# Kernel optimization log

Measured on AMD Instinct MI355X. Metric: run time of the kernel, lower is better.

Reference implementation:

```python
import jax, jax.numpy as jnp
import numpy as np

B, N, DIM = 4, 2048, 512
HEADS, DIM_HEAD = 8, 64
HID = HEADS * DIM_HEAD


def setup_inputs() -> dict:
    key = jax.random.key(0)
    k1, k2, k3, k4, k5 = jax.random.split(key, 5)
    x = jax.random.normal(k1, (B, N, DIM), jnp.float32)
    pos_bias = jax.random.normal(k2, (HEADS, N, N), jnp.float32) * 0.02
    focus_present_mask = jax.random.bernoulli(k3, 0.5, (B,))
    w_qkv = jax.random.normal(k4, (DIM, 3 * HID), jnp.float32) * (DIM ** -0.5)
    w_out = jax.random.normal(k5, (HID, DIM), jnp.float32) * (HID ** -0.5)
    return {"x": x, "pos_bias": pos_bias, "focus_present_mask": focus_present_mask,
            "w_qkv": w_qkv, "w_out": w_out}


def reference(x, pos_bias, focus_present_mask, w_qkv, w_out):
    scale = DIM_HEAD ** -0.5
    qkv = x @ w_qkv                                   # (B, N, 3*HID)
    q, k, v = jnp.split(qkv, 3, axis=-1)

    def to_heads(t):  # (B, N, HID) -> (B, H, N, D)
        return t.reshape(B, N, HEADS, DIM_HEAD).transpose(0, 2, 1, 3)

    q = to_heads(q) * scale
    k = to_heads(k)
    v = to_heads(v)

    sim = jnp.einsum('bhid,bhjd->bhij', q, k) + pos_bias[None]  # (B, H, N, N)

    # focus_present_mask[b] True -> attend only to self (eye); False -> attend all
    eye = jnp.eye(N, dtype=bool)
    mask = jnp.where(focus_present_mask[:, None, None, None],
                     eye[None, None], jnp.bool_(True))          # (B,1,N,N)
    sim = jnp.where(mask, sim, -jnp.finfo(sim.dtype).max)

    attn = jax.nn.softmax(sim, axis=-1)  # stable softmax == subtract-max + softmax
    out = jnp.einsum('bhij,bhjd->bhid', attn, v)
    out = out.transpose(0, 2, 1, 3).reshape(B, N, HID)
    return out @ w_out
```

## Files before the change

kernel.cpp:

```cpp
#include <hip/hip_runtime.h>
#include <hip/hip_bf16.h>
#include <float.h>

#define B_   4
#define N_   2048
#define DIM_ 512
#define H_   8
#define DH_  64

typedef unsigned short ushort;
typedef __attribute__((ext_vector_type(8))) short short8;
typedef __attribute__((ext_vector_type(4))) float f32x4;

__device__ __forceinline__ ushort f2bf(float f) {
    union { float f; unsigned u; } v; v.f = f;
    return (ushort)((v.u + 0x7fffu + ((v.u >> 16) & 1u)) >> 16);
}
__device__ __forceinline__ float bf2f(ushort u) {
    union { unsigned u; float f; } v; v.u = ((unsigned)u) << 16;
    return v.f;
}

typedef const __attribute__((address_space(1))) unsigned int* gas_t;
typedef __attribute__((address_space(3))) unsigned int* las_t;
__device__ __forceinline__ void gl_lds16(const void* g, void* l) {
    __builtin_amdgcn_global_load_lds((gas_t)g, (las_t)l, 16, 0, 0);
}

__global__ __launch_bounds__(256) void prep_kernel(
    const float* __restrict__ x, const float* __restrict__ wqkv,
    const float* __restrict__ wo,
    ushort* __restrict__ xb, ushort* __restrict__ wqkvT, ushort* __restrict__ woT)
{
    __shared__ ushort tile[64][72];
    const int bx = blockIdx.x;
    const int t = threadIdx.x;
    if (bx < 2048) {
        int gid = bx * 256 + t;
        const float4* xv = (const float4*)x;
        float4 v0 = xv[gid * 2], v1 = xv[gid * 2 + 1];
        uint4 pk;
        pk.x = (unsigned)f2bf(v0.x) | ((unsigned)f2bf(v0.y) << 16);
        pk.y = (unsigned)f2bf(v0.z) | ((unsigned)f2bf(v0.w) << 16);
        pk.z = (unsigned)f2bf(v1.x) | ((unsigned)f2bf(v1.y) << 16);
        pk.w = (unsigned)f2bf(v1.z) | ((unsigned)f2bf(v1.w) << 16);
        ((uint4*)xb)[gid] = pk;
        return;
    }
    int bi = bx - 2048;
    const float* src; ushort* dst; int C, tc, tr;
    if (bi < 192) { src = wqkv; dst = wqkvT; C = 1536; tc = bi % 24; tr = bi / 24; }
    else { bi -= 192; src = wo; dst = woT; C = 512; tc = bi & 7; tr = bi >> 3; }

    const int row = t >> 2, c16 = (t & 3) * 16;
    const float* sp = src + (size_t)(tr * 64 + row) * C + tc * 64 + c16;
    #pragma unroll
    for (int i = 0; i < 4; ++i) {
        float4 v = ((const float4*)sp)[i];
        tile[row][c16 + i * 4 + 0] = f2bf(v.x);
        tile[row][c16 + i * 4 + 1] = f2bf(v.y);
        tile[row][c16 + i * 4 + 2] = f2bf(v.z);
        tile[row][c16 + i * 4 + 3] = f2bf(v.w);
    }
    __syncthreads();
    ushort s[16];
    #pragma unroll
    for (int i = 0; i < 16; ++i) s[i] = tile[c16 + i][row];
    ushort* dp = dst + (size_t)(tc * 64 + row) * 512 + tr * 64 + c16;
    *(uint4*)dp       = *(uint4*)&s[0];
    *(uint4*)(dp + 8) = *(uint4*)&s[8];
}

__global__ __launch_bounds__(256) void qkv_gemm(
    const ushort* __restrict__ A, const ushort* __restrict__ Bt,
    const int* __restrict__ mask,
    ushort* __restrict__ qb, ushort* __restrict__ kb, ushort* __restrict__ vb,
    ushort* __restrict__ vT)
{
    __shared__ ushort sA[128 * 64];
    __shared__ ushort sB[128 * 64];
    const int bn = blockIdx.x;
    const int bm = blockIdx.y;
    if (bn < 8 && mask[bm >> 4] != 0) return;

    const int t = threadIdx.x, w_id = t >> 6, lane = t & 63;
    const int l15 = lane & 15, quad = lane >> 4;
    const int mo = (w_id & 1) * 64, no = (w_id >> 1) * 64;
    const int lr = lane >> 3, lc = (lane & 7) * 8;

    f32x4 acc[4][4] = {};

    for (int kt = 0; kt < 8; ++kt) {
        __syncthreads();
        #pragma unroll
        for (int i = 0; i < 4; ++i) {
            int j = w_id * 4 + i;
            gl_lds16(A  + (size_t)(bm * 128 + j * 8 + lr) * 512 + kt * 64 + lc, &sA[j * 512]);
            gl_lds16(Bt + (size_t)(bn * 128 + j * 8 + lr) * 512 + kt * 64 + lc, &sB[j * 512]);
        }
        __syncthreads();
        #pragma unroll
        for (int c = 0; c < 2; ++c) {
            short8 af[4], bf[4];
            #pragma unroll
            for (int mt = 0; mt < 4; ++mt)
                af[mt] = *(const short8*)&sA[(mo + mt * 16 + l15) * 64 + c * 32 + quad * 8];
            #pragma unroll
            for (int n2 = 0; n2 < 4; ++n2)
                bf[n2] = *(const short8*)&sB[(no + n2 * 16 + l15) * 64 + c * 32 + quad * 8];
            #pragma unroll
            for (int mt = 0; mt < 4; ++mt)
                #pragma unroll
                for (int n2 = 0; n2 < 4; ++n2)
                    acc[mt][n2] = __builtin_amdgcn_mfma_f32_16x16x32_bf16(af[mt], bf[n2], acc[mt][n2], 0, 0, 0);
        }
    }

    const int gn0 = bn * 128 + no;
    const int which = gn0 >> 9;
    const int h = (gn0 >> 6) & 7;
    ushort* dst = which == 0 ? qb : (which == 1 ? kb : vb);
    const float sc = which == 0 ? 0.125f : 1.0f;
    #pragma unroll
    for (int mt = 0; mt < 4; ++mt) {
        const int m0 = bm * 128 + mo + mt * 16 + quad * 4;
        #pragma unroll
        for (int n2 = 0; n2 < 4; ++n2) {
            int d = n2 * 16 + l15;
            ushort w0, w1, w2, w3;
            #pragma unroll
            for (int r = 0; r < 4; ++r) {
                int m = m0 + r, b = m >> 11, n = m & 2047;
                ushort bfv = f2bf(acc[mt][n2][r] * sc);
                dst[((size_t)(b * 8 + h) * 2048 + n) * 64 + d] = bfv;
                if (r == 0) w0 = bfv; else if (r == 1) w1 = bfv;
                else if (r == 2) w2 = bfv; else w3 = bfv;
            }
            if (which == 2) {
                int b = m0 >> 11, n0 = m0 & 2047;
                uint2 pk;
                pk.x = (unsigned)w0 | ((unsigned)w1 << 16);
                pk.y = (unsigned)w2 | ((unsigned)w3 << 16);
                *(uint2*)&vT[((size_t)(b * 8 + h) * 64 + d) * 2048 + n0] = pk;
            }
        }
    }
}

__global__ __launch_bounds__(256) void attn_kernel(
    const ushort* __restrict__ qg, const ushort* __restrict__ kg,
    const ushort* __restrict__ vTg, const float* __restrict__ bias,
    const int* __restrict__ mask,
    ushort* __restrict__ po, float* __restrict__ pl)
{
    const int bid = blockIdx.x;
    const int qblk = bid & 31, s = (bid >> 5) & 1, h = (bid >> 6) & 7, b = bid >> 9;
    if (mask[b] != 0) return;

    const int t = threadIdx.x, w_id = t >> 6, lane = t & 63;
    const int l15 = lane & 15, quad = lane >> 4;
    const int lr = lane >> 3, lc = (lane & 7) * 8;
    const int bh = b * 8 + h;
    const int kbase = s * 1024;

    __shared__ ushort lds_k[64 * 64];
    __shared__ ushort lds_vt[64 * 64];
    __shared__ ushort lds_sp[4 * 16 * 68];

    const ushort* kptr = kg  + (size_t)bh * 2048 * 64;
    const ushort* vtp  = vTg + (size_t)bh * 64 * 2048;

    const ushort* qrp = qg + (size_t)bh * 2048 * 64 + (size_t)(qblk * 64 + w_id * 16 + l15) * 64;
    short8 qf0 = *(const short8*)(qrp + quad * 8);
    short8 qf1 = *(const short8*)(qrp + 32 + quad * 8);

    const int qrow0 = qblk * 64 + w_id * 16 + quad * 4;
    const float* bp = bias + ((size_t)h * 2048 + qrow0) * 2048 + kbase;

    float breg[16];
    #pragma unroll
    for (int tt = 0; tt < 4; ++tt)
        #pragma unroll
        for (int r = 0; r < 4; ++r)
            breg[tt * 4 + r] = bp[(size_t)r * 2048 + tt * 16 + l15];

    f32x4 o[4] = {};
    float lsum[4] = {0.f, 0.f, 0.f, 0.f};

    for (int it = 0; it < 16; ++it) {
        __syncthreads();
        #pragma unroll
        for (int i = 0; i < 2; ++i) {
            int j = w_id * 2 + i;
            gl_lds16(kptr + (size_t)(kbase + it * 64 + j * 8 + lr) * 64 + lc, &lds_k[j * 512]);
            gl_lds16(vtp + (size_t)(j * 8 + lr) * 2048 + kbase + it * 64 + lc, &lds_vt[j * 512]);
        }
        __syncthreads();

        f32x4 sv[4] = {};
        #pragma unroll
        for (int tt = 0; tt < 4; ++tt) {
            short8 kf0 = *(const short8*)&lds_k[(tt * 16 + l15) * 64 + quad * 8];
            short8 kf1 = *(const short8*)&lds_k[(tt * 16 + l15) * 64 + 32 + quad * 8];
            sv[tt] = __builtin_amdgcn_mfma_f32_16x16x32_bf16(qf0, kf0, sv[tt], 0, 0, 0);
            sv[tt] = __builtin_amdgcn_mfma_f32_16x16x32_bf16(qf1, kf1, sv[tt], 0, 0, 0);
        }
        #pragma unroll
        for (int tt = 0; tt < 4; ++tt)
            #pragma unroll
            for (int r = 0; r < 4; ++r)
                sv[tt][r] += breg[tt * 4 + r];

        if (it < 15) {
            #pragma unroll
            for (int tt = 0; tt < 4; ++tt)
                #pragma unroll
                for (int r = 0; r < 4; ++r)
                    breg[tt * 4 + r] = bp[(size_t)r * 2048 + (it + 1) * 64 + tt * 16 + l15];
        }

        const int prow0 = (w_id * 16 + quad * 4) * 68;
        #pragma unroll
        for (int r = 0; r < 4; ++r) {
            float e0 = __expf(sv[0][r]), e1 = __expf(sv[1][r]);
            float e2 = __expf(sv[2][r]), e3 = __expf(sv[3][r]);
            lsum[r] += (e0 + e1) + (e2 + e3);
            const int pr = prow0 + r * 68;
            lds_sp[pr + l15]      = f2bf(e0);
            lds_sp[pr + 16 + l15] = f2bf(e1);
            lds_sp[pr + 32 + l15] = f2bf(e2);
            lds_sp[pr + 48 + l15] = f2bf(e3);
        }

        asm volatile("s_waitcnt lgkmcnt(0)" ::: "memory");

        short8 pf0 = *(const short8*)&lds_sp[(w_id * 16 + l15) * 68 + quad * 8];
        short8 pf1 = *(const short8*)&lds_sp[(w_id * 16 + l15) * 68 + 32 + quad * 8];
        #pragma unroll
        for (int nt = 0; nt < 4; ++nt) {
            short8 vf0 = *(const short8*)&lds_vt[(nt * 16 + l15) * 64 + quad * 8];
            short8 vf1 = *(const short8*)&lds_vt[(nt * 16 + l15) * 64 + 32 + quad * 8];
            o[nt] = __builtin_amdgcn_mfma_f32_16x16x32_bf16(pf0, vf0, o[nt], 0, 0, 0);
            o[nt] = __builtin_amdgcn_mfma_f32_16x16x32_bf16(pf1, vf1, o[nt], 0, 0, 0);
        }
    }

    #pragma unroll
    for (int r = 0; r < 4; ++r) {
        #pragma unroll
        for (int off = 1; off < 16; off <<= 1)
            lsum[r] += __shfl_xor(lsum[r], off, 64);
    }

    #pragma unroll
    for (int r = 0; r < 4; ++r) {
        const int qrow = qrow0 + r;
        const size_t base = ((size_t)(s * 32 + bh) * 2048 + qrow) * 64;
        #pragma unroll
        for (int nt = 0; nt < 4; ++nt)
            po[base + nt * 16 + l15] = f2bf(o[nt][r]);
        if (l15 == 0)
            pl[(size_t)(s * 32 + bh) * 2048 + qrow] = lsum[r];
    }
}

__global__ __launch_bounds__(256) void combine_kernel(
    const ushort* __restrict__ po, const float* __restrict__ pl,
    const ushort* __restrict__ vb, const int* __restrict__ mask,
    ushort* __restrict__ ob)
{
    const int gid = blockIdx.x * 256 + threadIdx.x;
    const int dd = (gid & 7) * 8;
    const int h = (gid >> 3) & 7, n = (gid >> 6) & 2047, b = gid >> 17;
    const int bh = b * 8 + h;
    ushort* op = ob + ((size_t)b * 2048 + n) * 512 + h * 64 + dd;
    if (mask[b] != 0) {
        *(uint4*)op = *(const uint4*)(vb + ((size_t)bh * 2048 + n) * 64 + dd);
        return;
    }
    const size_t i1 = (size_t)bh * 2048 + n;
    const size_t i2 = (size_t)(32 + bh) * 2048 + n;
    float inv = 1.f / (pl[i1] + pl[i2]);
    uint4 ua = *(const uint4*)(po + i1 * 64 + dd);
    uint4 ub = *(const uint4*)(po + i2 * 64 + dd);
    const ushort* pa = (const ushort*)&ua;
    const ushort* pb = (const ushort*)&ub;
    ushort res[8];
    #pragma unroll
    for (int j = 0; j < 8; ++j)
        res[j] = f2bf((bf2f(pa[j]) + bf2f(pb[j])) * inv);
    *(uint4*)op = *(uint4*)res;
}

__global__ __launch_bounds__(256) void out_gemm(
    const ushort* __restrict__ A, const ushort* __restrict__ Bt,
    float* __restrict__ out)
{
    __shared__ ushort sA[2][128 * 64];
    __shared__ ushort sB[2][128 * 64];
    const int bn = blockIdx.x;
    const int bm = blockIdx.y;
    const int t = threadIdx.x, w_id = t >> 6, lane = t & 63;
    const int l15 = lane & 15, quad = lane >> 4;
    const int mo = (w_id & 1) * 64, no = (w_id >> 1) * 64;
    const int lr = lane >> 3;
    const int lcs = ((lane & 7) ^ lr) * 8;
    const int rsw = l15 & 7;

    f32x4 acc[4][4] = {};

    #pragma unroll
    for (int i = 0; i < 4; ++i) {
        int j = w_id * 4 + i;
        gl_lds16(A  + (size_t)(bm * 128 + j * 8 + lr) * 512 + lcs, &sA[0][j * 512]);
        gl_lds16(Bt + (size_t)(bn * 128 + j * 8 + lr) * 512 + lcs, &sB[0][j * 512]);
    }
    asm volatile("s_waitcnt vmcnt(0)" ::: "memory");
    __syncthreads();

    for (int kt = 0; kt < 8; ++kt) {
        const int cur = kt & 1;
        if (kt + 1 < 8) {
            #pragma unroll
            for (int i = 0; i < 4; ++i) {
                int j = w_id * 4 + i;
                gl_lds16(A  + (size_t)(bm * 128 + j * 8 + lr) * 512 + (kt + 1) * 64 + lcs,
                         &sA[cur ^ 1][j * 512]);
                gl_lds16(Bt + (size_t)(bn * 128 + j * 8 + lr) * 512 + (kt + 1) * 64 + lcs,
                         &sB[cur ^ 1][j * 512]);
            }
        }
        #pragma unroll
        for (int c = 0; c < 2; ++c) {
            short8 af[4], bf[4];
            #pragma unroll
            for (int mt = 0; mt < 4; ++mt)
                af[mt] = *(const short8*)&sA[cur][(mo + mt * 16 + l15) * 64 + (((c * 4 + quad) ^ rsw)) * 8];
            #pragma unroll
            for (int n2 = 0; n2 < 4; ++n2)
                bf[n2] = *(const short8*)&sB[cur][(no + n2 * 16 + l15) * 64 + (((c * 4 + quad) ^ rsw)) * 8];
            #pragma unroll
            for (int mt = 0; mt < 4; ++mt)
                #pragma unroll
                for (int n2 = 0; n2 < 4; ++n2)
                    acc[mt][n2] = __builtin_amdgcn_mfma_f32_16x16x32_bf16(af[mt], bf[n2], acc[mt][n2], 0, 0, 0);
        }
        asm volatile("s_waitcnt vmcnt(0)" ::: "memory");
        __syncthreads();
    }
    #pragma unroll
    for (int mt = 0; mt < 4; ++mt) {
        const int m0 = bm * 128 + mo + mt * 16 + quad * 4;
        #pragma unroll
        for (int n2 = 0; n2 < 4; ++n2) {
            int col = bn * 128 + no + n2 * 16 + l15;
            #pragma unroll
            for (int r = 0; r < 4; ++r)
                out[(size_t)(m0 + r) * 512 + col] = acc[mt][n2][r];
        }
    }
}

extern "C" void kernel_launch(void* const* d_in, const int* in_sizes, int n_in,
                              void* d_out, int out_size, void* d_ws, size_t ws_size,
                              hipStream_t stream)
{
    const float* x        = (const float*)d_in[0];
    const float* pos_bias = (const float*)d_in[1];
    const int*   mask     = (const int*)d_in[2];
    const float* w_qkv    = (const float*)d_in[3];
    const float* w_out    = (const float*)d_in[4];
    float* out = (float*)d_out;

    char* ws = (char*)d_ws;
    ushort* qb    = (ushort*)(ws + 0);
    ushort* kb    = (ushort*)(ws + 8388608);
    ushort* vb    = (ushort*)(ws + 16777216);
    ushort* vT    = (ushort*)(ws + 25165824);
    ushort* xb    = (ushort*)(ws + 33554432);
    ushort* ob    = (ushort*)(ws + 33554432);
    ushort* po    = (ushort*)(ws + 41943040);
    float*  pl    = (float* )(ws + 58720256);
    ushort* woT   = (ushort*)(ws + 59244544);
    ushort* wqkvT = (ushort*)(ws + 59768832);

    prep_kernel<<<2304, 256, 0, stream>>>(x, w_qkv, w_out, xb, wqkvT, woT);
    qkv_gemm<<<dim3(12, 64), 256, 0, stream>>>(xb, wqkvT, mask, qb, kb, vb, vT);
    attn_kernel<<<2048, 256, 0, stream>>>(qb, kb, vT, pos_bias, mask, po, pl);
    combine_kernel<<<2048, 256, 0, stream>>>(po, pl, vb, mask, ob);
    out_gemm<<<dim3(4, 64), 256, 0, stream>>>(ob, woT, out);
}
```

Measured before the change: 292.2 us.

## Fuse split-KV combine into output GEMM and swizzle attention LDS tiles

The separate combine kernel is removed. The output GEMM now builds its A tile directly from the two partial attention outputs and their row sums, or from V for batches using the self-only mask. This drops a kernel launch and an intermediate write and read of the combined buffer, but the A tile is now computed redundantly by each of the 4 column blocks and the GEMM loses its double buffering. Separately, the attention kernel's K and V^T LDS tiles use an XOR column swizzle to reduce bank conflicts on fragment reads.

```diff
diff --git a/kernel.cpp b/kernel.cpp
--- a/kernel.cpp
+++ b/kernel.cpp
@@ -159,7 +159,9 @@
 
     const int t = threadIdx.x, w_id = t >> 6, lane = t & 63;
     const int l15 = lane & 15, quad = lane >> 4;
-    const int lr = lane >> 3, lc = (lane & 7) * 8;
+    const int lr = lane >> 3;
+    const int lcs = ((lane & 7) ^ lr) * 8;
+    const int rsw = l15 & 7;
     const int bh = b * 8 + h;
     const int kbase = s * 1024;
 
@@ -192,16 +194,17 @@
         #pragma unroll
         for (int i = 0; i < 2; ++i) {
             int j = w_id * 2 + i;
-            gl_lds16(kptr + (size_t)(kbase + it * 64 + j * 8 + lr) * 64 + lc, &lds_k[j * 512]);
-            gl_lds16(vtp + (size_t)(j * 8 + lr) * 2048 + kbase + it * 64 + lc, &lds_vt[j * 512]);
+            gl_lds16(kptr + (size_t)(kbase + it * 64 + j * 8 + lr) * 64 + lcs, &lds_k[j * 512]);
+            gl_lds16(vtp + (size_t)(j * 8 + lr) * 2048 + kbase + it * 64 + lcs, &lds_vt[j * 512]);
         }
         __syncthreads();
 
         f32x4 sv[4] = {};
         #pragma unroll
         for (int tt = 0; tt < 4; ++tt) {
-            short8 kf0 = *(const short8*)&lds_k[(tt * 16 + l15) * 64 + quad * 8];
-            short8 kf1 = *(const short8*)&lds_k[(tt * 16 + l15) * 64 + 32 + quad * 8];
+            const ushort* kr = &lds_k[(tt * 16 + l15) * 64];
+            short8 kf0 = *(const short8*)&kr[(quad ^ rsw) * 8];
+            short8 kf1 = *(const short8*)&kr[((4 + quad) ^ rsw) * 8];
             sv[tt] = __builtin_amdgcn_mfma_f32_16x16x32_bf16(qf0, kf0, sv[tt], 0, 0, 0);
             sv[tt] = __builtin_amdgcn_mfma_f32_16x16x32_bf16(qf1, kf1, sv[tt], 0, 0, 0);
         }
@@ -238,8 +241,9 @@
         short8 pf1 = *(const short8*)&lds_sp[(w_id * 16 + l15) * 68 + 32 + quad * 8];
         #pragma unroll
         for (int nt = 0; nt < 4; ++nt) {
-            short8 vf0 = *(const short8*)&lds_vt[(nt * 16 + l15) * 64 + quad * 8];
-            short8 vf1 = *(const short8*)&lds_vt[(nt * 16 + l15) * 64 + 32 + quad * 8];
+            const ushort* vr = &lds_vt[(nt * 16 + l15) * 64];
+            short8 vf0 = *(const short8*)&vr[(quad ^ rsw) * 8];
+            short8 vf1 = *(const short8*)&vr[((4 + quad) ^ rsw) * 8];
             o[nt] = __builtin_amdgcn_mfma_f32_16x16x32_bf16(pf0, vf0, o[nt], 0, 0, 0);
             o[nt] = __builtin_amdgcn_mfma_f32_16x16x32_bf16(pf1, vf1, o[nt], 0, 0, 0);
         }
@@ -264,89 +268,72 @@
     }
 }
 
-__global__ __launch_bounds__(256) void combine_kernel(
+__global__ __launch_bounds__(256) void out_gemm(
     const ushort* __restrict__ po, const float* __restrict__ pl,
     const ushort* __restrict__ vb, const int* __restrict__ mask,
-    ushort* __restrict__ ob)
-{
-    const int gid = blockIdx.x * 256 + threadIdx.x;
-    const int dd = (gid & 7) * 8;
-    const int h = (gid >> 3) & 7, n = (gid >> 6) & 2047, b = gid >> 17;
-    const int bh = b * 8 + h;
-    ushort* op = ob + ((size_t)b * 2048 + n) * 512 + h * 64 + dd;
-    if (mask[b] != 0) {
-        *(uint4*)op = *(const uint4*)(vb + ((size_t)bh * 2048 + n) * 64 + dd);
-        return;
-    }
-    const size_t i1 = (size_t)bh * 2048 + n;
-    const size_t i2 = (size_t)(32 + bh) * 2048 + n;
-    float inv = 1.f / (pl[i1] + pl[i2]);
-    uint4 ua = *(const uint4*)(po + i1 * 64 + dd);
-    uint4 ub = *(const uint4*)(po + i2 * 64 + dd);
-    const ushort* pa = (const ushort*)&ua;
-    const ushort* pb = (const ushort*)&ub;
-    ushort res[8];
-    #pragma unroll
-    for (int j = 0; j < 8; ++j)
-        res[j] = f2bf((bf2f(pa[j]) + bf2f(pb[j])) * inv);
-    *(uint4*)op = *(uint4*)res;
-}
-
-__global__ __launch_bounds__(256) void out_gemm(
-    const ushort* __restrict__ A, const ushort* __restrict__ Bt,
-    float* __restrict__ out)
-{
-    __shared__ ushort sA[2][128 * 64];
-    __shared__ ushort sB[2][128 * 64];
+    const ushort* __restrict__ Bt, float* __restrict__ out)
+{
+    __shared__ ushort sA[128 * 64];
+    __shared__ ushort sB[128 * 64];
     const int bn = blockIdx.x;
     const int bm = blockIdx.y;
     const int t = threadIdx.x, w_id = t >> 6, lane = t & 63;
     const int l15 = lane & 15, quad = lane >> 4;
     const int mo = (w_id & 1) * 64, no = (w_id >> 1) * 64;
-    const int lr = lane >> 3;
+    const int lr = lane >> 3, lc = (lane & 7) * 8;
     const int lcs = ((lane & 7) ^ lr) * 8;
     const int rsw = l15 & 7;
+    const int b = bm >> 4;
+    const int msk = mask[b];
 
     f32x4 acc[4][4] = {};
 
-    #pragma unroll
-    for (int i = 0; i < 4; ++i) {
-        int j = w_id * 4 + i;
-        gl_lds16(A  + (size_t)(bm * 128 + j * 8 + lr) * 512 + lcs, &sA[0][j * 512]);
-        gl_lds16(Bt + (size_t)(bn * 128 + j * 8 + lr) * 512 + lcs, &sB[0][j * 512]);
-    }
-    asm volatile("s_waitcnt vmcnt(0)" ::: "memory");
-    __syncthreads();
-
     for (int kt = 0; kt < 8; ++kt) {
-        const int cur = kt & 1;
-        if (kt + 1 < 8) {
-            #pragma unroll
-            for (int i = 0; i < 4; ++i) {
-                int j = w_id * 4 + i;
-                gl_lds16(A  + (size_t)(bm * 128 + j * 8 + lr) * 512 + (kt + 1) * 64 + lcs,
-                         &sA[cur ^ 1][j * 512]);
-                gl_lds16(Bt + (size_t)(bn * 128 + j * 8 + lr) * 512 + (kt + 1) * 64 + lcs,
-                         &sB[cur ^ 1][j * 512]);
+        __syncthreads();
+        #pragma unroll
+        for (int i = 0; i < 4; ++i) {
+            int j = w_id * 4 + i;
+            gl_lds16(Bt + (size_t)(bn * 128 + j * 8 + lr) * 512 + kt * 64 + lcs, &sB[j * 512]);
+        }
+        #pragma unroll
+        for (int i = 0; i < 4; ++i) {
+            int j = w_id * 4 + i;
+            int row = bm * 128 + j * 8 + lr;
+            int n = row & 2047;
+            ushort v8[8];
+            if (msk != 0) {
+                *(uint4*)v8 = *(const uint4*)&vb[((size_t)(b * 8 + kt) * 2048 + n) * 64 + lc];
+            } else {
+                const size_t i1 = (size_t)(b * 8 + kt) * 2048 + n;
+                const size_t i2 = (size_t)(32 + b * 8 + kt) * 2048 + n;
+                uint4 ua = *(const uint4*)&po[i1 * 64 + lc];
+                uint4 ub = *(const uint4*)&po[i2 * 64 + lc];
+                float inv = 1.f / (pl[i1] + pl[i2]);
+                const ushort* pa = (const ushort*)&ua;
+                const ushort* pb = (const ushort*)&ub;
+                #pragma unroll
+                for (int e = 0; e < 8; ++e)
+                    v8[e] = f2bf((bf2f(pa[e]) + bf2f(pb[e])) * inv);
             }
-        }
+            *(uint4*)&sA[j * 512 + lr * 64 + (((lane & 7) ^ lr)) * 8] = *(uint4*)v8;
+        }
+        __syncthreads();
+
         #pragma unroll
         for (int c = 0; c < 2; ++c) {
             short8 af[4], bf[4];
             #pragma unroll
             for (int mt = 0; mt < 4; ++mt)
-                af[mt] = *(const short8*)&sA[cur][(mo + mt * 16 + l15) * 64 + (((c * 4 + quad) ^ rsw)) * 8];
+                af[mt] = *(const short8*)&sA[(mo + mt * 16 + l15) * 64 + (((c * 4 + quad) ^ rsw)) * 8];
             #pragma unroll
             for (int n2 = 0; n2 < 4; ++n2)
-                bf[n2] = *(const short8*)&sB[cur][(no + n2 * 16 + l15) * 64 + (((c * 4 + quad) ^ rsw)) * 8];
+                bf[n2] = *(const short8*)&sB[(no + n2 * 16 + l15) * 64 + (((c * 4 + quad) ^ rsw)) * 8];
             #pragma unroll
             for (int mt = 0; mt < 4; ++mt)
                 #pragma unroll
                 for (int n2 = 0; n2 < 4; ++n2)
                     acc[mt][n2] = __builtin_amdgcn_mfma_f32_16x16x32_bf16(af[mt], bf[n2], acc[mt][n2], 0, 0, 0);
         }
-        asm volatile("s_waitcnt vmcnt(0)" ::: "memory");
-        __syncthreads();
     }
     #pragma unroll
     for (int mt = 0; mt < 4; ++mt) {
@@ -378,7 +365,6 @@
     ushort* vb    = (ushort*)(ws + 16777216);
     ushort* vT    = (ushort*)(ws + 25165824);
     ushort* xb    = (ushort*)(ws + 33554432);
-    ushort* ob    = (ushort*)(ws + 33554432);
     ushort* po    = (ushort*)(ws + 41943040);
     float*  pl    = (float* )(ws + 58720256);
     ushort* woT   = (ushort*)(ws + 59244544);
@@ -387,6 +373,5 @@
     prep_kernel<<<2304, 256, 0, stream>>>(x, w_qkv, w_out, xb, wqkvT, woT);
     qkv_gemm<<<dim3(12, 64), 256, 0, stream>>>(xb, wqkvT, mask, qb, kb, vb, vT);
     attn_kernel<<<2048, 256, 0, stream>>>(qb, kb, vT, pos_bias, mask, po, pl);
-    combine_kernel<<<2048, 256, 0, stream>>>(po, pl, vb, mask, ob);
-    out_gemm<<<dim3(4, 64), 256, 0, stream>>>(ob, woT, out);
-}
+    out_gemm<<<dim3(4, 64), 256, 0, stream>>>(po, pl, vb, mask, woT, out);
+}
```

Result: no change. 292.9 us (+0.2%).
